# Performance work log

Measured on AMD Instinct MI355X. Metric: run time of the kernel, lower is better.

## Reference

```python
import jax, jax.numpy as jnp
import numpy as np

B, S, D = 1, 2048, 2048
H, KVH, HD = 32, 8, 64  # head_dim = D // H
THETA = 10000.0
INIT_STD = 0.02


def _freqs_cos_sin(head_dim, end, theta):
    # precompute_freqs_cis, returned as (cos, sin) real tables [end, head_dim//2]
    freqs = 1.0 / theta ** (np.arange(0, head_dim, 2)[: head_dim // 2].astype(np.float32) / head_dim)
    t = np.arange(end)
    fr = np.outer(t, freqs).astype(np.float32)
    return jnp.asarray(np.cos(fr)), jnp.asarray(np.sin(fr))


def setup_inputs() -> dict:
    key = jax.random.key(0)
    ks = jax.random.split(key, 5)
    return {
        "hidden_states": jax.random.normal(ks[0], (B, S, D), jnp.float32),
        "wq": jax.random.normal(ks[1], (D, H * HD), jnp.float32) * INIT_STD,
        "wk": jax.random.normal(ks[2], (D, KVH * HD), jnp.float32) * INIT_STD,
        "wv": jax.random.normal(ks[3], (D, KVH * HD), jnp.float32) * INIT_STD,
        "wo": jax.random.normal(ks[4], (H * HD, D), jnp.float32) * INIT_STD,
        "position_ids": jnp.broadcast_to(jnp.arange(S, dtype=jnp.int32), (B, S)),
    }


def reference(hidden_states, wq, wk, wv, wo, position_ids):
    # QKV projections (no bias)
    xq = (hidden_states @ wq).reshape(B, S, H, HD)
    xk = (hidden_states @ wk).reshape(B, S, KVH, HD)
    xv = (hidden_states @ wv).reshape(B, S, KVH, HD)

    # rotary embedding: interleaved complex pairs over last dim
    cos_t, sin_t = _freqs_cos_sin(HD, S, THETA)        # [S, HD//2]
    cos = cos_t[position_ids][:, :, None, :]            # [B, S, 1, HD//2]
    sin = sin_t[position_ids][:, :, None, :]

    def rope(x):
        xr = x.astype(jnp.float32).reshape(*x.shape[:-1], -1, 2)
        a, b = xr[..., 0], xr[..., 1]
        # (a + i b) * (cos + i sin)
        ra = a * cos - b * sin
        rb = a * sin + b * cos
        return jnp.stack((ra, rb), axis=-1).reshape(x.shape)

    xq = rope(xq)
    xk = rope(xk)

    # GQA: repeat kv heads
    n_rep = H // KVH
    xk = jnp.repeat(xk[:, :, :, None, :], n_rep, axis=3).reshape(B, S, H, HD)
    xv = jnp.repeat(xv[:, :, :, None, :], n_rep, axis=3).reshape(B, S, H, HD)

    # causal masked softmax attention (full score matrix, as in dot_product_attention_weights)
    scores = jnp.einsum('bqhd,bkhd->bhqk', xq, xk) / np.float32(np.sqrt(HD))
    causal = jnp.tril(jnp.ones((S, S), dtype=bool))
    big_neg = jnp.finfo(jnp.float32).min
    scores = jnp.where(causal[None, None, :, :], scores, big_neg)
    attn = jax.nn.softmax(scores, axis=-1)

    out = jnp.einsum('bhqk,bkhd->bqhd', attn, xv).reshape(B, S, H * HD)
    return out @ wo
```

## Files before the change

kernel.cpp:

```cpp
#include <hip/hip_runtime.h>
#include <hip/hip_bf16.h>


using short8  = __attribute__((ext_vector_type(8))) short;
using f32x4   = __attribute__((ext_vector_type(4))) float;
using f32x16  = __attribute__((ext_vector_type(16))) float;
using f32x2   = __attribute__((ext_vector_type(2))) float;
using ushort4v= __attribute__((ext_vector_type(4))) unsigned short;

#define SEQ 2048
#define DIM 2048
#define NH  32
#define NKVH 8
#define HD  64
#define KVD 512
#define NQKV 3072

#define GLOAD_LDS16(g, l) \
  __builtin_amdgcn_global_load_lds((const __attribute__((address_space(1))) void*)(g), \
                                   (__attribute__((address_space(3))) void*)(l), 16, 0, 0)

__device__ __forceinline__ float bf2f(unsigned short u) {
  union { float f; unsigned v; } x; x.v = ((unsigned)u) << 16; return x.f;
}
__device__ __forceinline__ unsigned short f2bf(float f) {
  union { float f; unsigned v; } x; x.f = f;
  unsigned r = x.v + 0x7fffu + ((x.v >> 16) & 1u);
  return (unsigned short)(r >> 16);
}

__global__ __launch_bounds__(256) void k_cast(const float* __restrict__ src,
                                              unsigned short* __restrict__ dst, int n) {
  int idx = (blockIdx.x * 256 + threadIdx.x) * 4;
  if (idx < n) {
    f32x4 v = *(const f32x4*)(src + idx);
    ushort4v o;
    o[0] = f2bf(v[0]); o[1] = f2bf(v[1]); o[2] = f2bf(v[2]); o[3] = f2bf(v[3]);
    *(ushort4v*)(dst + idx) = o;
  }
}

__global__ __launch_bounds__(256) void k_tcast(const float* __restrict__ src, int C,
                                               unsigned short* __restrict__ dst) {
  __shared__ float tile[32][33];
  int c0 = blockIdx.x * 32, r0 = blockIdx.y * 32;
  int tx = threadIdx.x, ty = threadIdx.y;
  #pragma unroll
  for (int j = 0; j < 32; j += 8)
    tile[ty + j][tx] = src[(r0 + ty + j) * C + c0 + tx];
  __syncthreads();
  #pragma unroll
  for (int j = 0; j < 32; j += 8)
    dst[(c0 + ty + j) * 2048 + r0 + tx] = f2bf(tile[tx][ty + j]);
}

__global__ __launch_bounds__(256) void k_table(const int* __restrict__ pos,
                                               f32x2* __restrict__ tab) {
  int i = blockIdx.x * 256 + threadIdx.x;
  int s = i >> 5, p = i & 31;
  float freq = powf(10000.0f, -(float)(2 * p) / 64.0f);
  float ang = (float)pos[s] * freq;
  float sv, cv; sincosf(ang, &sv, &cv);
  f32x2 r; r[0] = cv; r[1] = sv;
  tab[i] = r;
}

template <int N, bool OUTF32>
__global__ __launch_bounds__(256) void k_gemm(const unsigned short* __restrict__ A,
                                              const unsigned short* __restrict__ Bt,
                                              void* __restrict__ Cout) {
  const int K = 2048;
  __shared__ unsigned short lA[128 * 64];
  __shared__ unsigned short lB[128 * 64];
  int m0 = blockIdx.y * 128, n0 = blockIdx.x * 128;
  int t = threadIdx.x, lane = t & 63, wid = t >> 6;
  int wr = wid >> 1, wc = wid & 1;
  int lr = lane & 15, lg = lane >> 4;

  f32x4 acc[4][4] = {};

  for (int k0 = 0; k0 < K; k0 += 64) {
    #pragma unroll
    for (int j = 0; j < 4; ++j) {
      int idx = t + 256 * j, row = idx >> 3, c8 = idx & 7;
      GLOAD_LDS16(A  + (m0 + row) * K + k0 + c8 * 8, lA + idx * 8);
      GLOAD_LDS16(Bt + (n0 + row) * K + k0 + c8 * 8, lB + idx * 8);
    }
    __syncthreads();
    #pragma unroll
    for (int kk = 0; kk < 64; kk += 32) {
      short8 af[4], bfr[4];
      #pragma unroll
      for (int i = 0; i < 4; ++i) {
        af[i]  = *(const short8*)(lA + (wr * 64 + i * 16 + lr) * 64 + kk + lg * 8);
        bfr[i] = *(const short8*)(lB + (wc * 64 + i * 16 + lr) * 64 + kk + lg * 8);
      }
      #pragma unroll
      for (int i = 0; i < 4; ++i)
        #pragma unroll
        for (int j = 0; j < 4; ++j)
          acc[i][j] = __builtin_amdgcn_mfma_f32_16x16x32_bf16(af[i], bfr[j], acc[i][j], 0, 0, 0);
    }
    __syncthreads();
  }
  #pragma unroll
  for (int i = 0; i < 4; ++i)
    #pragma unroll
    for (int j = 0; j < 4; ++j)
      #pragma unroll
      for (int r = 0; r < 4; ++r) {
        int row = m0 + wr * 64 + i * 16 + lg * 4 + r;
        int col = n0 + wc * 64 + j * 16 + lr;
        float v = acc[i][j][r];
        if constexpr (OUTF32) ((float*)Cout)[row * N + col] = v;
        else ((unsigned short*)Cout)[row * N + col] = f2bf(v);
      }
}

__global__ __launch_bounds__(256) void k_rope(const unsigned short* __restrict__ xqkv,
                                              const f32x2* __restrict__ tab,
                                              unsigned short* __restrict__ xq,
                                              unsigned short* __restrict__ xk) {
  int s = blockIdx.y;
  int j = blockIdx.x * 256 + threadIdx.x;
  bool isq = j < 1024;
  int col = isq ? (2 * j) : (DIM + 2 * (j - 1024));
  int p = (col >> 1) & 31;
  f32x2 cs = tab[s * 32 + p];
  unsigned both = *(const unsigned*)(xqkv + s * NQKV + col);
  float a = bf2f((unsigned short)(both & 0xffff));
  float b = bf2f((unsigned short)(both >> 16));
  float ra = a * cs[0] - b * cs[1];
  float rb = a * cs[1] + b * cs[0];
  if (isq) { ra *= 0.125f; rb *= 0.125f; }
  unsigned pk = (unsigned)f2bf(ra) | ((unsigned)f2bf(rb) << 16);
  if (isq) *(unsigned*)(xq + s * DIM + col) = pk;
  else     *(unsigned*)(xk + s * KVD + (col - DIM)) = pk;
}

__global__ __launch_bounds__(256) void k_vt(const unsigned short* __restrict__ xqkv,
                                            unsigned short* __restrict__ xvT) {
  __shared__ unsigned short tile[32][33];
  int c0 = blockIdx.x * 32, s0 = blockIdx.y * 32;
  int tx = threadIdx.x, ty = threadIdx.y;
  #pragma unroll
  for (int j = 0; j < 32; j += 8)
    tile[ty + j][tx] = xqkv[(s0 + ty + j) * NQKV + 2560 + c0 + tx];
  __syncthreads();
  #pragma unroll
  for (int j = 0; j < 32; j += 8)
    xvT[(c0 + ty + j) * SEQ + s0 + tx] = tile[tx][ty + j];
}

__global__ __launch_bounds__(256) void k_attn(const unsigned short* __restrict__ xq,
                                              const unsigned short* __restrict__ xk,
                                              const unsigned short* __restrict__ xvT,
                                              unsigned short* __restrict__ attnout) {
  int wid = threadIdx.x >> 6, lane = threadIdx.x & 63;
  int tid = blockIdx.x * 4 + wid;
  int h = tid >> 5, j = tid & 31;
  int kvh = h >> 2;
  int lq = lane & 31, hi = lane >> 5;

  #pragma unroll
  for (int ph = 0; ph < 2; ++ph) {
    int qb = ph ? (63 - j) : j;
    int q0 = qb * 32;

    short8 qf[4];
    #pragma unroll
    for (int s = 0; s < 4; ++s)
      qf[s] = *(const short8*)(xq + (q0 + lq) * DIM + h * HD + s * 16 + hi * 8);

    f32x16 o0 = {}, o1 = {};
    float m = -3.0e38f, l = 0.0f;

    for (int kv0 = 0; kv0 <= q0; kv0 += 32) {
      f32x16 st = {};
      #pragma unroll
      for (int s = 0; s < 4; ++s) {
        short8 kf = *(const short8*)(xk + (kv0 + lq) * KVD + kvh * HD + s * 16 + hi * 8);
        st = __builtin_amdgcn_mfma_f32_32x32x16_bf16(kf, qf[s], st, 0, 0, 0);
      }
      if (kv0 == q0) {
        #pragma unroll
        for (int r = 0; r < 16; ++r) {
          int kvl = (r & 3) + 8 * (r >> 2) + 4 * hi;
          if (kvl > lq) st[r] = -3.0e38f;
        }
      }
      float pmax = st[0];
      #pragma unroll
      for (int r = 1; r < 16; ++r) pmax = fmaxf(pmax, st[r]);
      pmax = fmaxf(pmax, __shfl_xor(pmax, 32));
      if (!__all(pmax - m <= 8.0f)) {
        float mnew = fmaxf(m, pmax);
        float scale = __expf(m - mnew);
        #pragma unroll
        for (int r = 0; r < 16; ++r) {
          int ql = (r & 3) + 8 * (r >> 2) + 4 * hi;
          float sc = __shfl(scale, ql);
          o0[r] *= sc; o1[r] *= sc;
        }
        l *= scale;
        m = mnew;
      }
      float p[16], sum = 0.0f;
      #pragma unroll
      for (int r = 0; r < 16; ++r) { p[r] = __expf(st[r] - m); sum += p[r]; }
      l += sum;
      unsigned w[8];
      #pragma unroll
      for (int i = 0; i < 8; ++i)
        asm("v_cvt_pk_bf16_f32 %0, %1, %2" : "=v"(w[i]) : "v"(p[2 * i]), "v"(p[2 * i + 1]));
      #pragma unroll
      for (int s2 = 0; s2 < 2; ++s2) {
        int b = s2 * 4;
        unsigned sw0 = __shfl_xor(w[b + 0], 32);
        unsigned sw1 = __shfl_xor(w[b + 1], 32);
        unsigned sw2 = __shfl_xor(w[b + 2], 32);
        unsigned sw3 = __shfl_xor(w[b + 3], 32);
        union { unsigned u[4]; short8 s8; } pa;
        pa.u[0] = hi ? sw2 : w[b + 0];
        pa.u[1] = hi ? sw3 : w[b + 1];
        pa.u[2] = hi ? w[b + 2] : sw0;
        pa.u[3] = hi ? w[b + 3] : sw1;
        short8 v0 = *(const short8*)(xvT + (kvh * HD + lq)      * SEQ + kv0 + s2 * 16 + hi * 8);
        short8 v1 = *(const short8*)(xvT + (kvh * HD + 32 + lq) * SEQ + kv0 + s2 * 16 + hi * 8);
        o0 = __builtin_amdgcn_mfma_f32_32x32x16_bf16(pa.s8, v0, o0, 0, 0, 0);
        o1 = __builtin_amdgcn_mfma_f32_32x32x16_bf16(pa.s8, v1, o1, 0, 0, 0);
      }
    }
    float lt = l + __shfl_xor(l, 32);
    float linv = 1.0f / lt;
    #pragma unroll
    for (int r = 0; r < 16; ++r) {
      int ql = (r & 3) + 8 * (r >> 2) + 4 * hi;
      float li = __shfl(linv, ql);
      int row = q0 + ql;
      attnout[row * DIM + h * HD + lq]      = f2bf(o0[r] * li);
      attnout[row * DIM + h * HD + 32 + lq] = f2bf(o1[r] * li);
    }
  }
}

extern "C" void kernel_launch(void* const* d_in, const int* in_sizes, int n_in,
                              void* d_out, int out_size, void* d_ws, size_t ws_size,
                              hipStream_t stream) {
  const float* hs = (const float*)d_in[0];
  const float* wq = (const float*)d_in[1];
  const float* wk = (const float*)d_in[2];
  const float* wv = (const float*)d_in[3];
  const float* wo = (const float*)d_in[4];
  const int* pos  = (const int*)d_in[5];
  float* out = (float*)d_out;

  char* ws = (char*)d_ws;
  unsigned short* wqkvT = (unsigned short*)(ws);
  unsigned short* woT   = (unsigned short*)(ws + 12582912);
  unsigned short* hbf   = (unsigned short*)(ws + 20971520);
  unsigned short* xqkv  = (unsigned short*)(ws + 29360128);
  unsigned short* xq    = (unsigned short*)(ws + 41943040);
  unsigned short* xk    = (unsigned short*)(ws + 50331648);
  unsigned short* xvT   = (unsigned short*)(ws + 52428800);
  f32x2*          tab   = (f32x2*)(ws + 54525952);
  unsigned short* attnout = hbf;

  k_cast<<<4096, 256, 0, stream>>>(hs, hbf, SEQ * DIM);
  k_tcast<<<dim3(64, 64), dim3(32, 8), 0, stream>>>(wq, 2048, wqkvT);
  k_tcast<<<dim3(16, 64), dim3(32, 8), 0, stream>>>(wk, 512, wqkvT + 2048 * 2048);
  k_tcast<<<dim3(16, 64), dim3(32, 8), 0, stream>>>(wv, 512, wqkvT + 2560 * 2048);
  k_tcast<<<dim3(64, 64), dim3(32, 8), 0, stream>>>(wo, 2048, woT);
  k_table<<<256, 256, 0, stream>>>(pos, tab);

  k_gemm<NQKV, false><<<dim3(NQKV / 128, SEQ / 128), 256, 0, stream>>>(hbf, wqkvT, xqkv);

  k_rope<<<dim3(5, SEQ), 256, 0, stream>>>(xqkv, tab, xq, xk);
  k_vt<<<dim3(16, 64), dim3(32, 8), 0, stream>>>(xqkv, xvT);

  k_attn<<<256, 256, 0, stream>>>(xq, xk, xvT, attnout);

  k_gemm<DIM, true><<<dim3(DIM / 128, SEQ / 128), 256, 0, stream>>>(attnout, woT, out);
}
```

Before: 296.0 us.

## Double-buffer GEMM with 8 waves, pipeline attention KV loads, use exp2 softmax

Measured after the change: 304.4 us. +2.9%, slower.

```diff
diff --git a/kernel.cpp b/kernel.cpp
--- a/kernel.cpp
+++ b/kernel.cpp
@@ -66,51 +66,62 @@
 }
 
 template <int N, bool OUTF32>
-__global__ __launch_bounds__(256) void k_gemm(const unsigned short* __restrict__ A,
+__global__ __launch_bounds__(512) void k_gemm(const unsigned short* __restrict__ A,
                                               const unsigned short* __restrict__ Bt,
                                               void* __restrict__ Cout) {
   const int K = 2048;
-  __shared__ unsigned short lA[128 * 64];
-  __shared__ unsigned short lB[128 * 64];
+  __shared__ unsigned short lA[2][128 * 64];
+  __shared__ unsigned short lB[2][128 * 64];
   int m0 = blockIdx.y * 128, n0 = blockIdx.x * 128;
   int t = threadIdx.x, lane = t & 63, wid = t >> 6;
-  int wr = wid >> 1, wc = wid & 1;
+  int wr = wid >> 2, wc = wid & 3;
   int lr = lane & 15, lg = lane >> 4;
 
-  f32x4 acc[4][4] = {};
-
+  f32x4 acc[4][2] = {};
+
+  auto stage = [&](int k0, int buf) {
+    #pragma unroll
+    for (int j = 0; j < 2; ++j) {
+      int idx = t + 512 * j, row = idx >> 3, c8 = idx & 7;
+      GLOAD_LDS16(A  + (m0 + row) * K + k0 + c8 * 8, &lA[buf][idx * 8]);
+      GLOAD_LDS16(Bt + (n0 + row) * K + k0 + c8 * 8, &lB[buf][idx * 8]);
+    }
+  };
+
+  stage(0, 0);
+  __syncthreads();
+  int cur = 0;
   for (int k0 = 0; k0 < K; k0 += 64) {
-    #pragma unroll
-    for (int j = 0; j < 4; ++j) {
-      int idx = t + 256 * j, row = idx >> 3, c8 = idx & 7;
-      GLOAD_LDS16(A  + (m0 + row) * K + k0 + c8 * 8, lA + idx * 8);
-      GLOAD_LDS16(Bt + (n0 + row) * K + k0 + c8 * 8, lB + idx * 8);
-    }
-    __syncthreads();
+    int kn = k0 + 64;
+    if (kn < K) stage(kn, cur ^ 1);
+    __builtin_amdgcn_s_setprio(1);
     #pragma unroll
     for (int kk = 0; kk < 64; kk += 32) {
-      short8 af[4], bfr[4];
-      #pragma unroll
-      for (int i = 0; i < 4; ++i) {
-        af[i]  = *(const short8*)(lA + (wr * 64 + i * 16 + lr) * 64 + kk + lg * 8);
-        bfr[i] = *(const short8*)(lB + (wc * 64 + i * 16 + lr) * 64 + kk + lg * 8);
-      }
+      short8 af[4], bfr[2];
+      #pragma unroll
+      for (int i = 0; i < 4; ++i)
+        af[i]  = *(const short8*)(&lA[cur][(wr * 64 + i * 16 + lr) * 64 + kk + lg * 8]);
+      #pragma unroll
+      for (int j = 0; j < 2; ++j)
+        bfr[j] = *(const short8*)(&lB[cur][(wc * 32 + j * 16 + lr) * 64 + kk + lg * 8]);
       #pragma unroll
       for (int i = 0; i < 4; ++i)
         #pragma unroll
-        for (int j = 0; j < 4; ++j)
+        for (int j = 0; j < 2; ++j)
           acc[i][j] = __builtin_amdgcn_mfma_f32_16x16x32_bf16(af[i], bfr[j], acc[i][j], 0, 0, 0);
     }
+    __builtin_amdgcn_s_setprio(0);
     __syncthreads();
+    cur ^= 1;
   }
   #pragma unroll
   for (int i = 0; i < 4; ++i)
     #pragma unroll
-    for (int j = 0; j < 4; ++j)
+    for (int j = 0; j < 2; ++j)
       #pragma unroll
       for (int r = 0; r < 4; ++r) {
         int row = m0 + wr * 64 + i * 16 + lg * 4 + r;
-        int col = n0 + wc * 64 + j * 16 + lr;
+        int col = n0 + wc * 32 + j * 16 + lr;
         float v = acc[i][j][r];
         if constexpr (OUTF32) ((float*)Cout)[row * N + col] = v;
         else ((unsigned short*)Cout)[row * N + col] = f2bf(v);
@@ -132,7 +143,8 @@
   float b = bf2f((unsigned short)(both >> 16));
   float ra = a * cs[0] - b * cs[1];
   float rb = a * cs[1] + b * cs[0];
-  if (isq) { ra *= 0.125f; rb *= 0.125f; }
+  const float QS = 0.125f * 1.44269504088896f;
+  if (isq) { ra *= QS; rb *= QS; }
   unsigned pk = (unsigned)f2bf(ra) | ((unsigned)f2bf(rb) << 16);
   if (isq) *(unsigned*)(xq + s * DIM + col) = pk;
   else     *(unsigned*)(xk + s * KVD + (col - DIM)) = pk;
@@ -157,90 +169,108 @@
                                               const unsigned short* __restrict__ xvT,
                                               unsigned short* __restrict__ attnout) {
   int wid = threadIdx.x >> 6, lane = threadIdx.x & 63;
-  int tid = blockIdx.x * 4 + wid;
-  int h = tid >> 5, j = tid & 31;
-  int kvh = h >> 2;
+  int kvh = blockIdx.x & 7;
+  int qb = 63 - (blockIdx.x >> 3);
+  int h = kvh * 4 + wid;
   int lq = lane & 31, hi = lane >> 5;
-
-  #pragma unroll
-  for (int ph = 0; ph < 2; ++ph) {
-    int qb = ph ? (63 - j) : j;
-    int q0 = qb * 32;
-
-    short8 qf[4];
+  int q0 = qb * 32;
+
+  short8 qf[4];
+  #pragma unroll
+  for (int s = 0; s < 4; ++s)
+    qf[s] = *(const short8*)(xq + (q0 + lq) * DIM + h * HD + s * 16 + hi * 8);
+
+  f32x16 o0 = {}, o1 = {};
+  float m = -3.0e38f, l = 0.0f;
+
+  auto loadK = [&](int kv0, short8* d) {
     #pragma unroll
     for (int s = 0; s < 4; ++s)
-      qf[s] = *(const short8*)(xq + (q0 + lq) * DIM + h * HD + s * 16 + hi * 8);
-
-    f32x16 o0 = {}, o1 = {};
-    float m = -3.0e38f, l = 0.0f;
-
-    for (int kv0 = 0; kv0 <= q0; kv0 += 32) {
-      f32x16 st = {};
-      #pragma unroll
-      for (int s = 0; s < 4; ++s) {
-        short8 kf = *(const short8*)(xk + (kv0 + lq) * KVD + kvh * HD + s * 16 + hi * 8);
-        st = __builtin_amdgcn_mfma_f32_32x32x16_bf16(kf, qf[s], st, 0, 0, 0);
+      d[s] = *(const short8*)(xk + (kv0 + lq) * KVD + kvh * HD + s * 16 + hi * 8);
+  };
+  auto loadV = [&](int kv0, short8* d) {
+    #pragma unroll
+    for (int s2 = 0; s2 < 2; ++s2) {
+      d[s2 * 2 + 0] = *(const short8*)(xvT + (kvh * HD + lq)      * SEQ + kv0 + s2 * 16 + hi * 8);
+      d[s2 * 2 + 1] = *(const short8*)(xvT + (kvh * HD + 32 + lq) * SEQ + kv0 + s2 * 16 + hi * 8);
+    }
+  };
+
+  short8 kf[4], vf[4];
+  loadK(0, kf); loadV(0, vf);
+
+  for (int kv0 = 0; kv0 <= q0; kv0 += 32) {
+    int kvn = min(kv0 + 32, q0);
+    short8 kn[4], vn[4];
+    loadK(kvn, kn); loadV(kvn, vn);
+
+    f32x16 st = {};
+    __builtin_amdgcn_s_setprio(1);
+    #pragma unroll
+    for (int s = 0; s < 4; ++s)
+      st = __builtin_amdgcn_mfma_f32_32x32x16_bf16(kf[s], qf[s], st, 0, 0, 0);
+    __builtin_amdgcn_s_setprio(0);
+
+    if (kv0 == q0) {
+      #pragma unroll
+      for (int r = 0; r < 16; ++r) {
+        int kvl = (r & 3) + 8 * (r >> 2) + 4 * hi;
+        if (kvl > lq) st[r] = -3.0e38f;
       }
-      if (kv0 == q0) {
-        #pragma unroll
-        for (int r = 0; r < 16; ++r) {
-          int kvl = (r & 3) + 8 * (r >> 2) + 4 * hi;
-          if (kvl > lq) st[r] = -3.0e38f;
-        }
+    }
+    float pmax = st[0];
+    #pragma unroll
+    for (int r = 1; r < 16; ++r) pmax = fmaxf(pmax, st[r]);
+    pmax = fmaxf(pmax, __shfl_xor(pmax, 32));
+    if (!__all(pmax - m <= 11.54f)) {
+      float mnew = fmaxf(m, pmax);
+      float scale = exp2f(m - mnew);
+      #pragma unroll
+      for (int r = 0; r < 16; ++r) {
+        int ql = (r & 3) + 8 * (r >> 2) + 4 * hi;
+        float sc = __shfl(scale, ql);
+        o0[r] *= sc; o1[r] *= sc;
       }
-      float pmax = st[0];
-      #pragma unroll
-      for (int r = 1; r < 16; ++r) pmax = fmaxf(pmax, st[r]);
-      pmax = fmaxf(pmax, __shfl_xor(pmax, 32));
-      if (!__all(pmax - m <= 8.0f)) {
-        float mnew = fmaxf(m, pmax);
-        float scale = __expf(m - mnew);
-        #pragma unroll
-        for (int r = 0; r < 16; ++r) {
-          int ql = (r & 3) + 8 * (r >> 2) + 4 * hi;
-          float sc = __shfl(scale, ql);
-          o0[r] *= sc; o1[r] *= sc;
-        }
-        l *= scale;
-        m = mnew;
-      }
-      float p[16], sum = 0.0f;
-      #pragma unroll
-      for (int r = 0; r < 16; ++r) { p[r] = __expf(st[r] - m); sum += p[r]; }
-      l += sum;
-      unsigned w[8];
-      #pragma unroll
-      for (int i = 0; i < 8; ++i)
-        asm("v_cvt_pk_bf16_f32 %0, %1, %2" : "=v"(w[i]) : "v"(p[2 * i]), "v"(p[2 * i + 1]));
-      #pragma unroll
-      for (int s2 = 0; s2 < 2; ++s2) {
-        int b = s2 * 4;
-        unsigned sw0 = __shfl_xor(w[b + 0], 32);
-        unsigned sw1 = __shfl_xor(w[b + 1], 32);
-        unsigned sw2 = __shfl_xor(w[b + 2], 32);
-        unsigned sw3 = __shfl_xor(w[b + 3], 32);
-        union { unsigned u[4]; short8 s8; } pa;
-        pa.u[0] = hi ? sw2 : w[b + 0];
-        pa.u[1] = hi ? sw3 : w[b + 1];
-        pa.u[2] = hi ? w[b + 2] : sw0;
-        pa.u[3] = hi ? w[b + 3] : sw1;
-        short8 v0 = *(const short8*)(xvT + (kvh * HD + lq)      * SEQ + kv0 + s2 * 16 + hi * 8);
-        short8 v1 = *(const short8*)(xvT + (kvh * HD + 32 + lq) * SEQ + kv0 + s2 * 16 + hi * 8);
-        o0 = __builtin_amdgcn_mfma_f32_32x32x16_bf16(pa.s8, v0, o0, 0, 0, 0);
-        o1 = __builtin_amdgcn_mfma_f32_32x32x16_bf16(pa.s8, v1, o1, 0, 0, 0);
-      }
-    }
-    float lt = l + __shfl_xor(l, 32);
-    float linv = 1.0f / lt;
-    #pragma unroll
-    for (int r = 0; r < 16; ++r) {
-      int ql = (r & 3) + 8 * (r >> 2) + 4 * hi;
-      float li = __shfl(linv, ql);
-      int row = q0 + ql;
-      attnout[row * DIM + h * HD + lq]      = f2bf(o0[r] * li);
-      attnout[row * DIM + h * HD + 32 + lq] = f2bf(o1[r] * li);
-    }
+      l *= scale;
+      m = mnew;
+    }
+    float p[16], sum = 0.0f;
+    #pragma unroll
+    for (int r = 0; r < 16; ++r) { p[r] = exp2f(st[r] - m); sum += p[r]; }
+    l += sum;
+    unsigned w[8];
+    #pragma unroll
+    for (int i = 0; i < 8; ++i)
+      asm("v_cvt_pk_bf16_f32 %0, %1, %2" : "=v"(w[i]) : "v"(p[2 * i]), "v"(p[2 * i + 1]));
+    __builtin_amdgcn_s_setprio(1);
+    #pragma unroll
+    for (int s2 = 0; s2 < 2; ++s2) {
+      int b = s2 * 4;
+      unsigned sw0 = __shfl_xor(w[b + 0], 32);
+      unsigned sw1 = __shfl_xor(w[b + 1], 32);
+      unsigned sw2 = __shfl_xor(w[b + 2], 32);
+      unsigned sw3 = __shfl_xor(w[b + 3], 32);
+      union { unsigned u[4]; short8 s8; } pa;
+      pa.u[0] = hi ? sw2 : w[b + 0];
+      pa.u[1] = hi ? sw3 : w[b + 1];
+      pa.u[2] = hi ? w[b + 2] : sw0;
+      pa.u[3] = hi ? w[b + 3] : sw1;
+      o0 = __builtin_amdgcn_mfma_f32_32x32x16_bf16(pa.s8, vf[s2 * 2 + 0], o0, 0, 0, 0);
+      o1 = __builtin_amdgcn_mfma_f32_32x32x16_bf16(pa.s8, vf[s2 * 2 + 1], o1, 0, 0, 0);
+    }
+    __builtin_amdgcn_s_setprio(0);
+    #pragma unroll
+    for (int s = 0; s < 4; ++s) { kf[s] = kn[s]; vf[s] = vn[s]; }
+  }
+  float lt = l + __shfl_xor(l, 32);
+  float linv = 1.0f / lt;
+  #pragma unroll
+  for (int r = 0; r < 16; ++r) {
+    int ql = (r & 3) + 8 * (r >> 2) + 4 * hi;
+    float li = __shfl(linv, ql);
+    int row = q0 + ql;
+    attnout[row * DIM + h * HD + lq]      = f2bf(o0[r] * li);
+    attnout[row * DIM + h * HD + 32 + lq] = f2bf(o1[r] * li);
   }
 }
 
@@ -273,12 +303,12 @@
   k_tcast<<<dim3(64, 64), dim3(32, 8), 0, stream>>>(wo, 2048, woT);
   k_table<<<256, 256, 0, stream>>>(pos, tab);
 
-  k_gemm<NQKV, false><<<dim3(NQKV / 128, SEQ / 128), 256, 0, stream>>>(hbf, wqkvT, xqkv);
+  k_gemm<NQKV, false><<<dim3(NQKV / 128, SEQ / 128), 512, 0, stream>>>(hbf, wqkvT, xqkv);
 
   k_rope<<<dim3(5, SEQ), 256, 0, stream>>>(xqkv, tab, xq, xk);
   k_vt<<<dim3(16, 64), dim3(32, 8), 0, stream>>>(xqkv, xvT);
 
-  k_attn<<<256, 256, 0, stream>>>(xq, xk, xvT, attnout);
-
-  k_gemm<DIM, true><<<dim3(DIM / 128, SEQ / 128), 256, 0, stream>>>(attnout, woT, out);
-}
+  k_attn<<<512, 256, 0, stream>>>(xq, xk, xvT, attnout);
+
+  k_gemm<DIM, true><<<dim3(DIM / 128, SEQ / 128), 512, 0, stream>>>(attnout, woT, out);
+}
```
